# Optimization experiments

Hardware: AMD Instinct MI355X
Metric: run time of the kernel (lower is better)

Reference implementation:

```python
import jax, jax.numpy as jnp
import numpy as np

N = 50000   # nodes
E = 640000  # edges
D = 128     # feature dim


def setup_inputs() -> dict:
    key = jax.random.key(0)
    k1, k2, k3, k4 = jax.random.split(key, 4)
    feat = jax.random.normal(k1, (N, D), dtype=jnp.float32)
    edge_weight = jax.random.normal(k2, (E,), dtype=jnp.float32)
    src = jax.random.randint(k3, (E,), 0, N)
    dst = jax.random.randint(k4, (E,), 0, N)
    beta = jnp.ones((1,), dtype=jnp.float32)   # learn_beta=True -> init 1
    eps = jnp.zeros((1,), dtype=jnp.float32)   # initial_eps = 0.0
    return {"feat": feat, "edge_weight": edge_weight, "src": src,
            "dst": dst, "beta": beta, "eps": eps}


def reference(feat, edge_weight, src, dst, beta, eps):
    n = feat.shape[0]
    # F.normalize(feat, p=2, dim=-1) with eps clamp
    norm = jnp.linalg.norm(feat, axis=-1, keepdims=True)
    norm_h = feat / jnp.maximum(norm, 1e-12)
    # e = beta * edge_weight, edge softmax grouped by SOURCE node (norm_by='src')
    e = beta[0] * edge_weight                               # [E]
    seg_max = jax.ops.segment_max(e, src, num_segments=n)   # [N]
    ex = jnp.exp(e - seg_max[src])                          # [E]
    seg_sum = jax.ops.segment_sum(ex, src, num_segments=n)  # [N]
    p = ex / seg_sum[src]                                   # [E]
    # message: u_mul_e(norm_h, p); reduce: sum at dst
    msg = norm_h[src] * p[:, None]                          # [E, D]
    h = jax.ops.segment_sum(msg, dst, num_segments=n)       # [N, D]
    return (1.0 + eps[0]) * feat + h
```

## Files before the change

kernel.cpp:

```cpp
#include <hip/hip_runtime.h>
#include <hip/hip_bf16.h>
#include <math.h>

#define FD 128
#define CAP 48
#define BSH 7
#define BINW 128
#define NBMAX 512
#define BCAP 2048
#define P2_BS 512
#define P2_K 8
#define P2_EPB 4096

typedef float v2f __attribute__((ext_vector_type(2)));

__device__ __forceinline__ float bf2f(unsigned u) { return __uint_as_float(u << 16); }
__device__ __forceinline__ unsigned f2bf(float f) {
    return (unsigned)__bfloat16_as_ushort(__float2bfloat16(f));
}

__global__ void __launch_bounds__(P2_BS) k_all(
        const float* __restrict__ ew, const int* __restrict__ src,
        const int* __restrict__ dst, const float* __restrict__ beta,
        const float* __restrict__ feat,
        int* __restrict__ cur_src, int* __restrict__ cur_dst,
        unsigned* __restrict__ reg_src,
        unsigned long long* __restrict__ reg_dst,
        unsigned short* __restrict__ f8,
        int e, int n, int sg) {
    __shared__ unsigned long long smem[P2_EPB];
    __shared__ int harr[4 * NBMAX];
    int b = blockIdx.x, t = threadIdx.x;
    int* h_cnt  = harr;
    int* h_base = harr + NBMAX;
    int* h_rank = harr + 2 * NBMAX;
    int* h_gbase= harr + 3 * NBMAX;

    if (b < sg) {
        unsigned* buf = (unsigned*)smem;
        h_cnt[t] = 0; h_rank[t] = 0;
        __syncthreads();
        int base0 = b * P2_EPB;
        float bb = beta[0];
        unsigned pay[P2_K]; int bn[P2_K];
        #pragma unroll
        for (int k = 0; k < P2_K; ++k) {
            int i = base0 + k * P2_BS + t;
            if (i < e) {
                int s = src[i];
                pay[k] = ((unsigned)s << 16) | f2bf(__expf(bb * ew[i]));
                bn[k] = s >> BSH;
                atomicAdd(&h_cnt[bn[k]], 1);
            } else bn[k] = -1;
        }
        __syncthreads();
        h_base[t] = h_cnt[t];
        __syncthreads();
        for (int off = 1; off < NBMAX; off <<= 1) {
            int v = (t >= off) ? h_base[t - off] : 0;
            __syncthreads(); h_base[t] += v; __syncthreads();
        }
        int excl = h_base[t] - h_cnt[t];
        __syncthreads();
        h_base[t] = excl;
        if (h_cnt[t] > 0) h_gbase[t] = atomicAdd(&cur_src[t], h_cnt[t]);
        __syncthreads();
        #pragma unroll
        for (int k = 0; k < P2_K; ++k) {
            if (bn[k] >= 0) {
                int r = atomicAdd(&h_rank[bn[k]], 1);
                buf[h_base[bn[k]] + r] = pay[k];
            }
        }
        __syncthreads();
        int tot = min(e - base0, P2_EPB);
        for (int p = t; p < tot; p += P2_BS) {
            unsigned q = buf[p];
            int b2 = (int)(q >> 16) >> BSH;
            int pos = h_gbase[b2] + (p - h_base[b2]);
            if (pos < BCAP) reg_src[(size_t)b2 * BCAP + pos] = q;
        }
    } else if (b < 2 * sg) {
        unsigned long long* buf = smem;
        h_cnt[t] = 0; h_rank[t] = 0;
        __syncthreads();
        int base0 = (b - sg) * P2_EPB;
        float bb = beta[0];
        unsigned long long pay[P2_K]; int bn[P2_K];
        #pragma unroll
        for (int k = 0; k < P2_K; ++k) {
            int i = base0 + k * P2_BS + t;
            if (i < e) {
                int s = src[i], d = dst[i];
                float ex = __expf(bb * ew[i]);
                pay[k] = ((unsigned long long)__float_as_uint(ex) << 32)
                       | ((unsigned long long)(unsigned)s << 16) | (unsigned)d;
                bn[k] = d >> BSH;
                atomicAdd(&h_cnt[bn[k]], 1);
            } else bn[k] = -1;
        }
        __syncthreads();
        h_base[t] = h_cnt[t];
        __syncthreads();
        for (int off = 1; off < NBMAX; off <<= 1) {
            int v = (t >= off) ? h_base[t - off] : 0;
            __syncthreads(); h_base[t] += v; __syncthreads();
        }
        int excl = h_base[t] - h_cnt[t];
        __syncthreads();
        h_base[t] = excl;
        if (h_cnt[t] > 0) h_gbase[t] = atomicAdd(&cur_dst[t], h_cnt[t]);
        __syncthreads();
        #pragma unroll
        for (int k = 0; k < P2_K; ++k) {
            if (bn[k] >= 0) {
                int r = atomicAdd(&h_rank[bn[k]], 1);
                buf[h_base[bn[k]] + r] = pay[k];
            }
        }
        __syncthreads();
        int tot = min(e - base0, P2_EPB);
        for (int p = t; p < tot; p += P2_BS) {
            unsigned long long qq = buf[p];
            int b2 = (int)(qq & 0xffffULL) >> BSH;
            int pos = h_gbase[b2] + (p - h_base[b2]);
            if (pos < BCAP) reg_dst[(size_t)b2 * BCAP + pos] = qq;
        }
    } else {
        int row  = (b - 2 * sg) * (P2_BS >> 6) + (t >> 6);
        int lane = t & 63;
        if (row >= n) return;
        float2 v = reinterpret_cast<const float2*>(feat + (size_t)row * FD)[lane];
        float s = v.x * v.x + v.y * v.y;
        #pragma unroll
        for (int m = 32; m >= 1; m >>= 1) s += __shfl_xor(s, m, 64);
        float inv = 1.0f / fmaxf(sqrtf(s), 1e-12f);
        unsigned pk = __builtin_amdgcn_cvt_pk_fp8_f32(v.x * inv, v.y * inv, 0, false);
        f8[(size_t)row * 64 + lane] = (unsigned short)(pk & 0xffffu);
    }
}

__global__ void __launch_bounds__(256) k_seg_reduce(
        const int* __restrict__ cur_src,
        const unsigned* __restrict__ reg_src,
        float* __restrict__ rcp_seg, int n) {
    __shared__ float acc[BINW];
    int b = blockIdx.x, t = threadIdx.x;
    if (t < BINW) acc[t] = 0.0f;
    __syncthreads();
    int cnt = min(cur_src[b], BCAP);
    const unsigned* base = reg_src + (size_t)b * BCAP;
    for (int i = t; i < cnt; i += 256) {
        unsigned p = base[i];
        atomicAdd(&acc[(p >> 16) & (BINW - 1)], bf2f(p & 0xffffu));
    }
    __syncthreads();
    int row = b * BINW + t;
    if (t < BINW && row < n)
        rcp_seg[row] = 1.0f / acc[t];
}

__global__ void __launch_bounds__(512) k_gather(
        const float* __restrict__ feat,
        const unsigned short* __restrict__ f8,
        const float* __restrict__ rcp_seg,
        const int* __restrict__ cur_dst,
        const unsigned long long* __restrict__ reg_dst,
        const float* __restrict__ eps,
        float* __restrict__ out, int n) {
    __shared__ unsigned lp[64 * CAP];
    __shared__ int lc[64];
    int hb = blockIdx.x;
    int b = hb >> 1, half = hb & 1;
    int t = threadIdx.x;
    if (t < 64) lc[t] = 0;
    __syncthreads();
    int cnt_all = min(cur_dst[b], BCAP);
    const unsigned long long* base = reg_dst + (size_t)b * BCAP;
    for (int i = t; i < cnt_all; i += 512) {
        unsigned long long qq = base[i];
        int dl = (int)(qq & (unsigned long long)(BINW - 1));
        if ((dl >> 6) == half) {
            unsigned sv  = (unsigned)((qq >> 16) & 0xffffULL);
            unsigned exb = f2bf(__uint_as_float((unsigned)(qq >> 32)));
            int slot = atomicAdd(&lc[dl & 63], 1);
            if (slot < CAP) lp[(dl & 63) * CAP + slot] = (sv << 16) | exb;
        }
    }
    __syncthreads();
    int wv = t >> 6, lane = t & 63, q = lane >> 4, li = lane & 15;
    float c0 = 1.0f + eps[0];
    for (int rr = 0; rr < 8; ++rr) {
        int r = wv * 8 + rr;
        int row = b * BINW + half * 64 + r;
        if (row >= n) break;
        int cnt = min(lc[r], CAP);
        float acc[8];
        #pragma unroll
        for (int i = 0; i < 8; ++i) acc[i] = 0.0f;
        if (q == 0) {
            float4 f0 = reinterpret_cast<const float4*>(feat + (size_t)row * FD)[li * 2];
            float4 f1 = reinterpret_cast<const float4*>(feat + (size_t)row * FD)[li * 2 + 1];
            acc[0] = c0 * f0.x; acc[1] = c0 * f0.y; acc[2] = c0 * f0.z; acc[3] = c0 * f0.w;
            acc[4] = c0 * f1.x; acc[5] = c0 * f1.y; acc[6] = c0 * f1.z; acc[7] = c0 * f1.w;
        }
        int sv = 0; float cv = 0.0f;
        if (lane < cnt) {
            unsigned pr = lp[r * CAP + lane];
            sv = (int)(pr >> 16);
            cv = bf2f(pr & 0xffffu) * rcp_seg[sv];
        }
        for (int j = 0; j < cnt; j += 4) {
            int idx = j + q;
            int   ss = __shfl(sv, idx, 64);
            float cc = __shfl(cv, idx, 64);
            if (idx < cnt) {
                uint2 w = reinterpret_cast<const uint2*>(f8 + (size_t)ss * 64)[li];
                v2f p0 = __builtin_amdgcn_cvt_pk_f32_fp8(w.x, false);
                v2f p1 = __builtin_amdgcn_cvt_pk_f32_fp8(w.x, true);
                v2f p2 = __builtin_amdgcn_cvt_pk_f32_fp8(w.y, false);
                v2f p3 = __builtin_amdgcn_cvt_pk_f32_fp8(w.y, true);
                acc[0] = fmaf(cc, p0.x, acc[0]);
                acc[1] = fmaf(cc, p0.y, acc[1]);
                acc[2] = fmaf(cc, p1.x, acc[2]);
                acc[3] = fmaf(cc, p1.y, acc[3]);
                acc[4] = fmaf(cc, p2.x, acc[4]);
                acc[5] = fmaf(cc, p2.y, acc[5]);
                acc[6] = fmaf(cc, p3.x, acc[6]);
                acc[7] = fmaf(cc, p3.y, acc[7]);
            }
        }
        #pragma unroll
        for (int i = 0; i < 8; ++i) {
            acc[i] += __shfl_xor(acc[i], 16, 64);
            acc[i] += __shfl_xor(acc[i], 32, 64);
        }
        if (q == 0) {
            float4* orow = reinterpret_cast<float4*>(out + (size_t)row * FD);
            orow[li * 2]     = make_float4(acc[0], acc[1], acc[2], acc[3]);
            orow[li * 2 + 1] = make_float4(acc[4], acc[5], acc[6], acc[7]);
        }
    }
}


__global__ void k_fused(const float* __restrict__ ew,
                        const int* __restrict__ src,
                        const int* __restrict__ dst,
                        const float* __restrict__ beta,
                        const float* __restrict__ feat,
                        float* __restrict__ seg_sum,
                        int* __restrict__ cursor,
                        unsigned* __restrict__ pairs,
                        unsigned* __restrict__ fb16,
                        int cap, int e, int n, int eb) {
    int b = blockIdx.x;
    if (b < eb) {
        int base = (b * blockDim.x + threadIdx.x) * 4;
        if (base >= e) return;
        float bb = beta[0];
        if (base + 4 <= e) {
            int4   s4 = *reinterpret_cast<const int4*>(src + base);
            int4   d4 = *reinterpret_cast<const int4*>(dst + base);
            float4 w4 = *reinterpret_cast<const float4*>(ew + base);
            float ex0 = __expf(bb * w4.x), ex1 = __expf(bb * w4.y);
            float ex2 = __expf(bb * w4.z), ex3 = __expf(bb * w4.w);
            unsafeAtomicAdd(&seg_sum[s4.x], ex0);
            unsafeAtomicAdd(&seg_sum[s4.y], ex1);
            unsafeAtomicAdd(&seg_sum[s4.z], ex2);
            unsafeAtomicAdd(&seg_sum[s4.w], ex3);
            int sl0 = atomicAdd(&cursor[d4.x], 1);
            int sl1 = atomicAdd(&cursor[d4.y], 1);
            int sl2 = atomicAdd(&cursor[d4.z], 1);
            int sl3 = atomicAdd(&cursor[d4.w], 1);
            if (sl0 < cap) pairs[(size_t)d4.x * cap + sl0] = ((unsigned)s4.x << 16) | f2bf(ex0);
            if (sl1 < cap) pairs[(size_t)d4.y * cap + sl1] = ((unsigned)s4.y << 16) | f2bf(ex1);
            if (sl2 < cap) pairs[(size_t)d4.z * cap + sl2] = ((unsigned)s4.z << 16) | f2bf(ex2);
            if (sl3 < cap) pairs[(size_t)d4.w * cap + sl3] = ((unsigned)s4.w << 16) | f2bf(ex3);
        } else {
            for (int i = base; i < e; ++i) {
                int s = src[i], d = dst[i];
                float ex = __expf(bb * ew[i]);
                unsafeAtomicAdd(&seg_sum[s], ex);
                int slot = atomicAdd(&cursor[d], 1);
                if (slot < cap) pairs[(size_t)d * cap + slot] = ((unsigned)s << 16) | f2bf(ex);
            }
        }
    } else {
        int row  = (b - eb) * (blockDim.x >> 6) + (threadIdx.x >> 6);
        int lane = threadIdx.x & 63;
        if (row >= n) return;
        float2 v = reinterpret_cast<const float2*>(feat + (size_t)row * FD)[lane];
        float s = v.x * v.x + v.y * v.y;
        #pragma unroll
        for (int m = 32; m >= 1; m >>= 1) s += __shfl_xor(s, m, 64);
        float inv = 1.0f / fmaxf(sqrtf(s), 1e-12f);
        fb16[(size_t)row * 64 + lane] = (f2bf(v.y * inv) << 16) | f2bf(v.x * inv);
    }
}

__global__ void __launch_bounds__(256) k_gather_p(const float* __restrict__ feat,
                                                  const unsigned* __restrict__ fb16,
                                                  const float* __restrict__ seg_sum,
                                                  const int* __restrict__ cursor,
                                                  const unsigned* __restrict__ pairs,
                                                  const float* __restrict__ eps,
                                                  float* __restrict__ out,
                                                  int cap, int n) {
    int row  = blockIdx.x * (blockDim.x >> 6) + (threadIdx.x >> 6);
    int lane = threadIdx.x & 63;
    if (row >= n) return;
    int q  = lane >> 4;
    int li = lane & 15;
    int cnt = min(cursor[row], cap);
    float acc[8];
    #pragma unroll
    for (int i = 0; i < 8; ++i) acc[i] = 0.0f;
    if (q == 0) {
        float c0 = 1.0f + eps[0];
        float4 f0 = reinterpret_cast<const float4*>(feat + (size_t)row * FD)[li * 2];
        float4 f1 = reinterpret_cast<const float4*>(feat + (size_t)row * FD)[li * 2 + 1];
        acc[0] = c0 * f0.x; acc[1] = c0 * f0.y; acc[2] = c0 * f0.z; acc[3] = c0 * f0.w;
        acc[4] = c0 * f1.x; acc[5] = c0 * f1.y; acc[6] = c0 * f1.z; acc[7] = c0 * f1.w;
    }
    size_t beg = (size_t)row * cap;
    for (int k = 0; k < cnt; k += 64) {
        int m = min(64, cnt - k);
        int sv = 0; float cv = 0.0f;
        if (lane < m) {
            unsigned pr = pairs[beg + k + lane];
            sv = (int)(pr >> 16);
            cv = bf2f(pr & 0xffffu) / seg_sum[sv];
        }
        for (int j = 0; j < m; j += 4) {
            int idx = j + q;
            int   ss = __shfl(sv, idx, 64);
            float cc = __shfl(cv, idx, 64);
            if (idx < m) {
                uint4 w = reinterpret_cast<const uint4*>(fb16 + (size_t)ss * 64)[li];
                acc[0] = fmaf(cc, bf2f(w.x & 0xffffu), acc[0]);
                acc[1] = fmaf(cc, bf2f(w.x >> 16),     acc[1]);
                acc[2] = fmaf(cc, bf2f(w.y & 0xffffu), acc[2]);
                acc[3] = fmaf(cc, bf2f(w.y >> 16),     acc[3]);
                acc[4] = fmaf(cc, bf2f(w.z & 0xffffu), acc[4]);
                acc[5] = fmaf(cc, bf2f(w.z >> 16),     acc[5]);
                acc[6] = fmaf(cc, bf2f(w.w & 0xffffu), acc[6]);
                acc[7] = fmaf(cc, bf2f(w.w >> 16),     acc[7]);
            }
        }
    }
    #pragma unroll
    for (int i = 0; i < 8; ++i) {
        acc[i] += __shfl_xor(acc[i], 16, 64);
        acc[i] += __shfl_xor(acc[i], 32, 64);
    }
    if (q == 0) {
        float4* orow = reinterpret_cast<float4*>(out + (size_t)row * FD);
        orow[li * 2]     = make_float4(acc[0], acc[1], acc[2], acc[3]);
        orow[li * 2 + 1] = make_float4(acc[4], acc[5], acc[6], acc[7]);
    }
}


extern "C" void kernel_launch(void* const* d_in, const int* in_sizes, int n_in,
                              void* d_out, int out_size, void* d_ws, size_t ws_size,
                              hipStream_t stream) {
    const float* feat = (const float*)d_in[0];
    const float* ew   = (const float*)d_in[1];
    const int*   src  = (const int*)d_in[2];
    const int*   dst  = (const int*)d_in[3];
    const float* beta = (const float*)d_in[4];
    const float* eps  = (const float*)d_in[5];
    float* out = (float*)d_out;

    const int n = in_sizes[0] / FD;
    const int e = in_sizes[1];

    const int nb = (n + BINW - 1) >> BSH;

    size_t need_bin = (size_t)nb * BCAP * 8 + (size_t)nb * BCAP * 4 + (size_t)n * 4
                    + (size_t)(2 * nb) * 4 + (size_t)n * FD;

    if (n <= 65535 && nb <= NBMAX && ws_size >= need_bin) {
        unsigned long long* reg_dst = (unsigned long long*)d_ws;
        unsigned* reg_src = (unsigned*)(reg_dst + (size_t)nb * BCAP);
        float*    rcp_seg = (float*)(reg_src + (size_t)nb * BCAP);
        int*      cur_src = (int*)(rcp_seg + n);
        int*      cur_dst = cur_src + nb;
        unsigned short* f8 = (unsigned short*)(cur_dst + nb);

        hipMemsetAsync(cur_src, 0, (size_t)(2 * nb) * 4, stream);
        int sg = (e + P2_EPB - 1) / P2_EPB;
        int sb = (n + (P2_BS / 64) - 1) / (P2_BS / 64);
        k_all<<<2 * sg + sb, P2_BS, 0, stream>>>(ew, src, dst, beta, feat,
                                                 cur_src, cur_dst, reg_src, reg_dst,
                                                 f8, e, n, sg);
        k_seg_reduce<<<nb, 256, 0, stream>>>(cur_src, reg_src, rcp_seg, n);
        k_gather<<<2 * nb, 512, 0, stream>>>(feat, f8, rcp_seg, cur_dst, reg_dst,
                                             eps, out, n);
    } else {
        const int rpb   = 256 / 64;
        const int ngrid = (n + rpb - 1) / rpb;
        const int eb    = ((e + 3) / 4 + 255) / 256;
        size_t fixed  = (size_t)n * 4 * 2;
        size_t fb16_b = (size_t)n * FD * 2;
        int cap = (ws_size >= (size_t)n * 64 * 4 + fixed + fb16_b) ? 64 : 48;

        unsigned* pairs   = (unsigned*)d_ws;
        float*    seg_sum = (float*)(pairs + (size_t)n * cap);
        int*      cursor  = (int*)(seg_sum + n);
        unsigned* fb16    = (unsigned*)(cursor + n);

        hipMemsetAsync(seg_sum, 0, fixed, stream);
        k_fused<<<eb + ngrid, 256, 0, stream>>>(ew, src, dst, beta, feat,
                                                seg_sum, cursor, pairs, fb16,
                                                4, e, n, eb);
        k_gather_p<<<ngrid, 256, 0, stream>>>(feat, fb16, seg_sum, cursor, pairs,
                                              eps, out, cap, n);
    }
}
```

Baseline: 64.20 us.

## Use wave-shuffle scan for bin offsets and move feature normalization into segment-reduce kernel

The per-block 512-entry exclusive scan over bin counts, which used a Hillis-Steele loop with two barriers per step, is replaced by a wavefront shuffle scan combined with a small cross-wave prefix, leaving far fewer block-wide barriers. The feature L2-normalize/fp8 pack blocks move out of the scatter kernel and into the segment-sum kernel, which now runs with 512 threads. This rebalances work across the two launches so the scatter kernel is lighter. The fallback path also now passes cap instead of a hardcoded 4, which looks like a fix.

```diff
diff --git a/kernel.cpp b/kernel.cpp
--- a/kernel.cpp
+++ b/kernel.cpp
@@ -19,22 +19,36 @@
     return (unsigned)__bfloat16_as_ushort(__float2bfloat16(f));
 }
 
-__global__ void __launch_bounds__(P2_BS) k_all(
+__device__ __forceinline__ int wave_excl_scan(int cnt, int t, int* wsum) {
+    int lane = t & 63, wv = t >> 6;
+    int x = cnt;
+    #pragma unroll
+    for (int d = 1; d < 64; d <<= 1) {
+        int y = __shfl_up(x, d, 64);
+        if (lane >= d) x += y;
+    }
+    if (lane == 63) wsum[wv] = x;
+    __syncthreads();
+    if (t == 0) {
+        int a = 0;
+        #pragma unroll
+        for (int j = 0; j < 8; ++j) { int tp = wsum[j]; wsum[j] = a; a += tp; }
+    }
+    __syncthreads();
+    return x - cnt + wsum[wv];
+}
+
+__global__ void __launch_bounds__(P2_BS) k_scatter2(
         const float* __restrict__ ew, const int* __restrict__ src,
         const int* __restrict__ dst, const float* __restrict__ beta,
-        const float* __restrict__ feat,
         int* __restrict__ cur_src, int* __restrict__ cur_dst,
         unsigned* __restrict__ reg_src,
         unsigned long long* __restrict__ reg_dst,
-        unsigned short* __restrict__ f8,
-        int e, int n, int sg) {
+        int e, int sg) {
     __shared__ unsigned long long smem[P2_EPB];
-    __shared__ int harr[4 * NBMAX];
+    __shared__ int h_cnt[NBMAX], h_base[NBMAX], h_rank[NBMAX], h_gbase[NBMAX];
+    __shared__ int wsum[8];
     int b = blockIdx.x, t = threadIdx.x;
-    int* h_cnt  = harr;
-    int* h_base = harr + NBMAX;
-    int* h_rank = harr + 2 * NBMAX;
-    int* h_gbase= harr + 3 * NBMAX;
 
     if (b < sg) {
         unsigned* buf = (unsigned*)smem;
@@ -54,16 +68,10 @@
             } else bn[k] = -1;
         }
         __syncthreads();
-        h_base[t] = h_cnt[t];
-        __syncthreads();
-        for (int off = 1; off < NBMAX; off <<= 1) {
-            int v = (t >= off) ? h_base[t - off] : 0;
-            __syncthreads(); h_base[t] += v; __syncthreads();
-        }
-        int excl = h_base[t] - h_cnt[t];
-        __syncthreads();
+        int cnt = h_cnt[t];
+        int excl = wave_excl_scan(cnt, t, wsum);
         h_base[t] = excl;
-        if (h_cnt[t] > 0) h_gbase[t] = atomicAdd(&cur_src[t], h_cnt[t]);
+        if (cnt > 0) h_gbase[t] = atomicAdd(&cur_src[t], cnt);
         __syncthreads();
         #pragma unroll
         for (int k = 0; k < P2_K; ++k) {
@@ -80,7 +88,7 @@
             int pos = h_gbase[b2] + (p - h_base[b2]);
             if (pos < BCAP) reg_src[(size_t)b2 * BCAP + pos] = q;
         }
-    } else if (b < 2 * sg) {
+    } else {
         unsigned long long* buf = smem;
         h_cnt[t] = 0; h_rank[t] = 0;
         __syncthreads();
@@ -100,16 +108,10 @@
             } else bn[k] = -1;
         }
         __syncthreads();
-        h_base[t] = h_cnt[t];
-        __syncthreads();
-        for (int off = 1; off < NBMAX; off <<= 1) {
-            int v = (t >= off) ? h_base[t - off] : 0;
-            __syncthreads(); h_base[t] += v; __syncthreads();
-        }
-        int excl = h_base[t] - h_cnt[t];
-        __syncthreads();
+        int cnt = h_cnt[t];
+        int excl = wave_excl_scan(cnt, t, wsum);
         h_base[t] = excl;
-        if (h_cnt[t] > 0) h_gbase[t] = atomicAdd(&cur_dst[t], h_cnt[t]);
+        if (cnt > 0) h_gbase[t] = atomicAdd(&cur_dst[t], cnt);
         __syncthreads();
         #pragma unroll
         for (int k = 0; k < P2_K; ++k) {
@@ -126,8 +128,33 @@
             int pos = h_gbase[b2] + (p - h_base[b2]);
             if (pos < BCAP) reg_dst[(size_t)b2 * BCAP + pos] = qq;
         }
+    }
+}
+
+__global__ void __launch_bounds__(P2_BS) k_mid(
+        const int* __restrict__ cur_src,
+        const unsigned* __restrict__ reg_src,
+        const float* __restrict__ feat,
+        float* __restrict__ rcp_seg,
+        unsigned short* __restrict__ f8,
+        int n, int nb) {
+    int b = blockIdx.x, t = threadIdx.x;
+    if (b < nb) {
+        __shared__ float acc[BINW];
+        if (t < BINW) acc[t] = 0.0f;
+        __syncthreads();
+        int cnt = min(cur_src[b], BCAP);
+        const unsigned* base = reg_src + (size_t)b * BCAP;
+        for (int i = t; i < cnt; i += P2_BS) {
+            unsigned p = base[i];
+            atomicAdd(&acc[(p >> 16) & (BINW - 1)], bf2f(p & 0xffffu));
+        }
+        __syncthreads();
+        int row = b * BINW + t;
+        if (t < BINW && row < n)
+            rcp_seg[row] = 1.0f / acc[t];
     } else {
-        int row  = (b - 2 * sg) * (P2_BS >> 6) + (t >> 6);
+        int row  = (b - nb) * (P2_BS >> 6) + (t >> 6);
         int lane = t & 63;
         if (row >= n) return;
         float2 v = reinterpret_cast<const float2*>(feat + (size_t)row * FD)[lane];
@@ -138,26 +165,6 @@
         unsigned pk = __builtin_amdgcn_cvt_pk_fp8_f32(v.x * inv, v.y * inv, 0, false);
         f8[(size_t)row * 64 + lane] = (unsigned short)(pk & 0xffffu);
     }
-}
-
-__global__ void __launch_bounds__(256) k_seg_reduce(
-        const int* __restrict__ cur_src,
-        const unsigned* __restrict__ reg_src,
-        float* __restrict__ rcp_seg, int n) {
-    __shared__ float acc[BINW];
-    int b = blockIdx.x, t = threadIdx.x;
-    if (t < BINW) acc[t] = 0.0f;
-    __syncthreads();
-    int cnt = min(cur_src[b], BCAP);
-    const unsigned* base = reg_src + (size_t)b * BCAP;
-    for (int i = t; i < cnt; i += 256) {
-        unsigned p = base[i];
-        atomicAdd(&acc[(p >> 16) & (BINW - 1)], bf2f(p & 0xffffu));
-    }
-    __syncthreads();
-    int row = b * BINW + t;
-    if (t < BINW && row < n)
-        rcp_seg[row] = 1.0f / acc[t];
 }
 
 __global__ void __launch_bounds__(512) k_gather(
@@ -392,10 +399,10 @@
         hipMemsetAsync(cur_src, 0, (size_t)(2 * nb) * 4, stream);
         int sg = (e + P2_EPB - 1) / P2_EPB;
         int sb = (n + (P2_BS / 64) - 1) / (P2_BS / 64);
-        k_all<<<2 * sg + sb, P2_BS, 0, stream>>>(ew, src, dst, beta, feat,
+        k_scatter2<<<2 * sg, P2_BS, 0, stream>>>(ew, src, dst, beta,
                                                  cur_src, cur_dst, reg_src, reg_dst,
-                                                 f8, e, n, sg);
-        k_seg_reduce<<<nb, 256, 0, stream>>>(cur_src, reg_src, rcp_seg, n);
+                                                 e, sg);
+        k_mid<<<nb + sb, P2_BS, 0, stream>>>(cur_src, reg_src, feat, rcp_seg, f8, n, nb);
         k_gather<<<2 * nb, 512, 0, stream>>>(feat, f8, rcp_seg, cur_dst, reg_dst,
                                              eps, out, n);
     } else {
@@ -414,7 +421,7 @@
         hipMemsetAsync(seg_sum, 0, fixed, stream);
         k_fused<<<eb + ngrid, 256, 0, stream>>>(ew, src, dst, beta, feat,
                                                 seg_sum, cursor, pairs, fb16,
-                                                4, e, n, eb);
+                                                cap, e, n, eb);
         k_gather_p<<<ngrid, 256, 0, stream>>>(feat, fb16, seg_sum, cursor, pairs,
                                               eps, out, cap, n);
     }
```

Result: slower. 67.29 us (+4.8%).
